# Performance work log

Measured on AMD Instinct MI355X. Metric: run time of the kernel, lower is better.

The kernel has to match this reference:

```python
import jax, jax.numpy as jnp
import numpy as np

DIM = 512
NUM_GROUPS = 32
HEADS = 16
HEAD_DIM = 32
EPS = 1e-6


def group_norm(x, w, b, num_groups=NUM_GROUPS, eps=EPS):
    # x: [B, C, H, W]
    B, C, H, W = x.shape
    xg = x.reshape(B, num_groups, -1)
    mean = xg.mean(axis=-1, keepdims=True)
    var = xg.var(axis=-1, keepdims=True)
    xg = (xg - mean) / jnp.sqrt(var + eps)
    x = xg.reshape(B, C, H, W)
    return x * w[None, :, None, None] + b[None, :, None, None]


def conv1x1(x, w, b):
    # x: [B, C, H, W], w: [O, C], b: [O]
    return jnp.einsum('bchw,oc->bohw', x, w) + b[None, :, None, None]


def setup_inputs() -> dict:
    key = jax.random.key(0)
    ks = jax.random.split(key, 12)
    s = 1.0 / np.sqrt(DIM)
    d = {
        'x': jax.random.normal(ks[0], (1, DIM, 64, 64), dtype=jnp.float32),
        'gn_w': jnp.ones((DIM,), dtype=jnp.float32),
        'gn_b': jnp.zeros((DIM,), dtype=jnp.float32),
        'wq': jax.random.normal(ks[1], (DIM, DIM), dtype=jnp.float32) * s,
        'bq': jax.random.normal(ks[2], (DIM,), dtype=jnp.float32) * 0.01,
        'wk': jax.random.normal(ks[3], (DIM, DIM), dtype=jnp.float32) * s,
        'bk': jax.random.normal(ks[4], (DIM,), dtype=jnp.float32) * 0.01,
        'wv': jax.random.normal(ks[5], (DIM, DIM), dtype=jnp.float32) * s,
        'bv': jax.random.normal(ks[6], (DIM,), dtype=jnp.float32) * 0.01,
        'wo': jax.random.normal(ks[7], (DIM, DIM), dtype=jnp.float32) * s,
        'bo': jax.random.normal(ks[8], (DIM,), dtype=jnp.float32) * 0.01,
    }
    return d


def reference(x, gn_w, gn_b, wq, bq, wk, bk, wv, bv, wo, bo):
    B, C, H, W = x.shape
    N = H * W
    scale = HEAD_DIM ** -0.5

    q_in = x
    qn = group_norm(x, gn_w, gn_b)
    # Faithful to source: v-branch applies norm_q to the already-normalized q.
    vn = group_norm(qn, gn_w, gn_b)

    q = conv1x1(qn, wq, bq)
    k = conv1x1(vn, wk, bk)
    v = conv1x1(vn, wv, bv)

    def to_tokens(t):
        # [B, C, H, W] -> [B, heads, N, head_dim]
        return t.reshape(B, HEADS, HEAD_DIM, N).transpose(0, 1, 3, 2)

    q, k, v = to_tokens(q), to_tokens(k), to_tokens(v)

    attn = jax.nn.softmax(jnp.einsum('bhnd,bhmd->bhnm', q, k) * scale, axis=-1)
    out = jnp.einsum('bhnm,bhmd->bhnd', attn, v)  # [B, heads, N, head_dim]
    out = out.transpose(0, 1, 3, 2).reshape(B, C, H, W)
    out = conv1x1(out, wo, bo)
    return (out + q_in) / jnp.sqrt(jnp.float32(2.0))
```

## Files before the change

### kernel.cpp

```cpp
#include <hip/hip_runtime.h>

#define NTOK 4096
#define CHAN 512
#define GSIZE 65536
#define RSQRT2 0.7071067811865476f
#define SCALEX 0.2550348837f
#define WB_OFF 32768
#define QT_OFF (WB_OFF + 2097152)
#define XT_OFF (QT_OFF + 4194304)
#define WS_NEEDED ((size_t)(XT_OFF + 4194304))

typedef unsigned short ushort_t;
typedef __attribute__((ext_vector_type(8))) short bf16x8;
typedef __attribute__((ext_vector_type(8))) _Float16 f16x8;
typedef __attribute__((ext_vector_type(4))) float f32x4;

__device__ __forceinline__ ushort_t f2b(float f) {
    unsigned u = __float_as_uint(f);
    unsigned r = (u + 0x7FFFu + ((u >> 16) & 1u)) >> 16;
    return (ushort_t)r;
}
__device__ __forceinline__ unsigned pack2r(float a, float b) {
    unsigned ua = __float_as_uint(a), ub = __float_as_uint(b);
    return ((ua + 0x8000u) >> 16) | ((ub + 0x8000u) & 0xFFFF0000u);
}
__device__ __forceinline__ unsigned packh2(float a, float b) {
    return __builtin_bit_cast(unsigned, __builtin_amdgcn_cvt_pkrtz(a, b));
}
__device__ __forceinline__ ushort_t f2h(float f) {
    return (ushort_t)(packh2(f, f) & 0xFFFFu);
}
__device__ __forceinline__ bf16x8 ldfrag(const ushort_t* p) {
    return __builtin_bit_cast(bf16x8, *(const uint4*)p);
}
__device__ __forceinline__ f16x8 ldfragh(const ushort_t* p) {
    return __builtin_bit_cast(f16x8, *(const uint4*)p);
}
__device__ __forceinline__ float exp2_raw(float x) {
#if __has_builtin(__builtin_amdgcn_exp2f)
    return __builtin_amdgcn_exp2f(x);
#else
    return __expf(x * 0.6931471805599453f);
#endif
}
__device__ __forceinline__ void ldg2lds16(const void* g, void* l) {
    __builtin_amdgcn_global_load_lds(
        (const __attribute__((address_space(1))) void*)g,
        (__attribute__((address_space(3))) void*)l, 16, 0, 0);
}

__global__ void diag_kernel(float* out, float v) {
    if (threadIdx.x == 0 && blockIdx.x == 0) out[0] = v;
}

__global__ __launch_bounds__(256) void gn_sums(const float* __restrict__ x,
                                               float* __restrict__ S,
                                               float* __restrict__ SS) {
    int c = blockIdx.x, t = threadIdx.x;
    const float4* p = (const float4*)(x + (size_t)c * 4096);
    float s = 0.f, ss = 0.f;
    #pragma unroll
    for (int i = 0; i < 4; i++) {
        float4 f = p[i * 256 + t];
        s += f.x + f.y + f.z + f.w;
        ss += f.x * f.x + f.y * f.y + f.z * f.z + f.w * f.w;
    }
    #pragma unroll
    for (int off = 32; off > 0; off >>= 1) {
        s += __shfl_xor(s, off);
        ss += __shfl_xor(ss, off);
    }
    __shared__ float as[4], bs[4];
    int w = t >> 6;
    if ((t & 63) == 0) { as[w] = s; bs[w] = ss; }
    __syncthreads();
    if (t == 0) {
        S[c] = as[0] + as[1] + as[2] + as[3];
        SS[c] = bs[0] + bs[1] + bs[2] + bs[3];
    }
}

__global__ __launch_bounds__(512) void gn_coef(const float* __restrict__ S,
                                               const float* __restrict__ SS,
                                               const float* __restrict__ gnw,
                                               const float* __restrict__ gnb,
                                               float* __restrict__ qa,
                                               float* __restrict__ qd,
                                               float* __restrict__ va,
                                               float* __restrict__ vd) {
    int c = threadIdx.x;
    float Sc = S[c], SSc = SS[c];
    float gs = Sc, gss = SSc;
    #pragma unroll
    for (int off = 1; off < 16; off <<= 1) {
        gs += __shfl_xor(gs, off);
        gss += __shfl_xor(gss, off);
    }
    float mu = gs * (1.f / GSIZE);
    float var = gss * (1.f / GSIZE) - mu * mu;
    float r1 = rsqrtf(var + 1e-6f);
    float wc = gnw[c], bc = gnb[c];
    float a1 = r1 * wc;
    float d1 = bc - mu * a1;
    qa[c] = a1; qd[c] = d1;
    float S2 = a1 * Sc + 4096.f * d1;
    float SS2 = a1 * a1 * SSc + 2.f * a1 * d1 * Sc + 4096.f * d1 * d1;
    float gs2 = S2, gss2 = SS2;
    #pragma unroll
    for (int off = 1; off < 16; off <<= 1) {
        gs2 += __shfl_xor(gs2, off);
        gss2 += __shfl_xor(gss2, off);
    }
    float mu2 = gs2 * (1.f / GSIZE);
    float var2 = gss2 * (1.f / GSIZE) - mu2 * mu2;
    float r2 = rsqrtf(var2 + 1e-6f);
    float a2 = r2 * wc;
    va[c] = a1 * a2;
    vd[c] = a2 * (d1 - mu2) + bc;
}

__global__ __launch_bounds__(256) void prep_all(const float* __restrict__ wq,
                                                const float* __restrict__ wk,
                                                const float* __restrict__ wv,
                                                const float* __restrict__ wo,
                                                const float* __restrict__ bq,
                                                const float* __restrict__ bk,
                                                const float* __restrict__ bv,
                                                const float* __restrict__ qa,
                                                const float* __restrict__ qd,
                                                const float* __restrict__ va,
                                                const float* __restrict__ vd,
                                                float* __restrict__ bqf,
                                                float* __restrict__ bkf,
                                                float* __restrict__ bvf,
                                                ushort_t* __restrict__ Wb) {
    int bx = blockIdx.x;
    if (bx < 384) {
        int row = bx * 4 + (threadIdx.x >> 6);
        int lane = threadIdx.x & 63;
        int m = row >> 9;
        int o = row & 511;
        const float* W = (m == 0) ? wq : (m == 1) ? wk : wv;
        const float* b = (m == 0) ? bq : (m == 1) ? bk : bv;
        const float* d = (m == 0) ? qd : vd;
        float* outp    = (m == 0) ? bqf : (m == 1) ? bkf : bvf;
        const float4* wr = (const float4*)(W + (size_t)o * 512) + lane * 2;
        const float4* dr = (const float4*)d + lane * 2;
        float4 a0 = wr[0], a1 = wr[1], d0 = dr[0], d1 = dr[1];
        float acc = a0.x * d0.x + a0.y * d0.y + a0.z * d0.z + a0.w * d0.w
                  + a1.x * d1.x + a1.y * d1.y + a1.z * d1.z + a1.w * d1.w;
        #pragma unroll
        for (int off = 32; off > 0; off >>= 1) acc += __shfl_xor(acc, off);
        if (lane == 0) outp[o] = b[o] + acc;
    } else {
        int idx = bx - 384;
        int y = idx >> 8;
        const float* src = (y == 0) ? wq : (y == 1) ? wk : (y == 2) ? wv : wo;
        int i = ((idx & 255) * 256 + threadIdx.x) * 4;
        float4 f = *(const float4*)(src + i);
        if (y < 3) {
            const float* aff = (y == 0) ? qa : va;
            float4 a = *(const float4*)(aff + (i & 511));
            f.x *= a.x; f.y *= a.y; f.z *= a.z; f.w *= a.w;
        }
        uint2 u;
        u.x = pack2r(f.x, f.y);
        u.y = pack2r(f.z, f.w);
        *(uint2*)(Wb + (size_t)y * 262144 + i) = u;
    }
}

__global__ __launch_bounds__(256) void xprep(const float* __restrict__ x,
                                             ushort_t* __restrict__ xT) {
    int bx = blockIdx.x;
    int t0 = (bx & 63) << 6;
    int c0 = (bx >> 6) << 6;
    int t = threadIdx.x;
    int tok = t & 63, c16 = t >> 6;
    float v[16];
    #pragma unroll
    for (int i = 0; i < 16; i++)
        v[i] = x[(size_t)(c0 + c16 * 16 + i) * NTOK + t0 + tok];
    uint4 u0, u1;
    u0.x = pack2r(v[0], v[1]);   u0.y = pack2r(v[2], v[3]);
    u0.z = pack2r(v[4], v[5]);   u0.w = pack2r(v[6], v[7]);
    u1.x = pack2r(v[8], v[9]);   u1.y = pack2r(v[10], v[11]);
    u1.z = pack2r(v[12], v[13]); u1.w = pack2r(v[14], v[15]);
    ushort_t* dst = xT + (size_t)(t0 + tok) * 512 + c0 + c16 * 16;
    *(uint4*)dst = u0;
    *(uint4*)(dst + 8) = u1;
}

__global__ __launch_bounds__(256) void qkv_mfma(const ushort_t* __restrict__ xT,
                                                const ushort_t* __restrict__ Wb,
                                                const float* __restrict__ bqf,
                                                const float* __restrict__ bkf,
                                                const float* __restrict__ bvf,
                                                ushort_t* __restrict__ QT,
                                                ushort_t* __restrict__ KT,
                                                ushort_t* __restrict__ Vb) {
    __shared__ __align__(16) ushort_t SH[2][12288];
    int t = threadIdx.x;
    int nbase = blockIdx.x << 6;
    int y = blockIdx.y;
    int buf = y >> 2;
    int obase = (y & 3) << 7;
    const ushort_t* Wsrc = Wb + (size_t)buf * 262144 + (size_t)obase * 512;
    const float* bias = (buf == 0) ? bqf : (buf == 1) ? bkf : bvf;

    int w = t >> 6, lane = t & 63, q15 = lane & 15, quad = lane >> 4;
    f32x4 acc[2][4];
    #pragma unroll
    for (int i = 0; i < 2; i++)
        #pragma unroll
        for (int j = 0; j < 4; j++) acc[i][j] = (f32x4){0.f, 0.f, 0.f, 0.f};

    auto issue = [&](int ck, int b) {
        ushort_t* base = SH[b];
        #pragma unroll
        for (int i = 0; i < 4; i++) {
            int idx = t + (i << 8);
            int row = idx >> 3, gs = idx & 7;
            int g = gs ^ (row & 7);
            ldg2lds16(&Wsrc[(size_t)row * 512 + ck + g * 8], &base[idx * 8]);
        }
        #pragma unroll
        for (int i = 0; i < 2; i++) {
            int idx = t + (i << 8);
            int tok = idx >> 3, gs = idx & 7;
            int g = gs ^ (tok & 7);
            ldg2lds16(&xT[(size_t)(nbase + tok) * 512 + ck + g * 8],
                      &base[8192 + idx * 8]);
        }
    };

    issue(0, 0);
    int swz = q15 & 7;
    for (int s = 0; s < 8; s++) {
        int cur = s & 1;
        __syncthreads();
        if (s < 7) issue((s + 1) * 64, cur ^ 1);
        const ushort_t* Wl = SH[cur];
        const ushort_t* Bn = SH[cur] + 8192;
        #pragma unroll
        for (int kk = 0; kk < 2; kk++) {
            int g = (kk * 4 + quad) ^ swz;
            bf16x8 af0 = ldfrag(&Wl[((w * 32 + q15) * 8 + g) * 8]);
            bf16x8 af1 = ldfrag(&Wl[((w * 32 + 16 + q15) * 8 + g) * 8]);
            #pragma unroll
            for (int n8 = 0; n8 < 4; n8++) {
                bf16x8 bfv = ldfrag(&Bn[((n8 * 16 + q15) * 8 + g) * 8]);
                acc[0][n8] = __builtin_amdgcn_mfma_f32_16x16x32_bf16(af0, bfv, acc[0][n8], 0, 0, 0);
                acc[1][n8] = __builtin_amdgcn_mfma_f32_16x16x32_bf16(af1, bfv, acc[1][n8], 0, 0, 0);
            }
        }
    }

    if (buf == 2) {
        #pragma unroll
        for (int mi = 0; mi < 2; mi++)
            #pragma unroll
            for (int r = 0; r < 4; r++) {
                int o = obase + w * 32 + mi * 16 + quad * 4 + r;
                float bo = bias[o];
                #pragma unroll
                for (int n8 = 0; n8 < 4; n8++)
                    Vb[(size_t)o * NTOK + nbase + n8 * 16 + q15] = f2h(acc[mi][n8][r] + bo);
            }
        return;
    }

    ushort_t* Tl = SH[0];
    __syncthreads();
    float qs = (buf == 0) ? SCALEX : 1.0f;
    #pragma unroll
    for (int mi = 0; mi < 2; mi++)
        #pragma unroll
        for (int r = 0; r < 4; r++) {
            int mloc = w * 32 + mi * 16 + quad * 4 + r;
            float bo = bias[obase + mloc];
            #pragma unroll
            for (int n8 = 0; n8 < 4; n8++)
                Tl[(n8 * 16 + q15) * 136 + mloc] = f2b((acc[mi][n8][r] + bo) * qs);
        }
    __syncthreads();
    ushort_t* dstT = (buf == 0) ? QT : KT;
    #pragma unroll
    for (int i = 0; i < 4; i++) {
        int idx = 4 * t + i;
        int row = idx >> 4, ch = idx & 15;
        uint4 u = *(const uint4*)&Tl[row * 136 + ch * 8];
        *(uint4*)&dstT[(size_t)(nbase + row) * 512 + obase + ch * 8] = u;
    }
}

__global__ __launch_bounds__(512, 4) void attn_v14(ushort_t* __restrict__ QT,
                                                   const ushort_t* __restrict__ KT,
                                                   const ushort_t* __restrict__ V) {
    __shared__ __align__(16) ushort_t KtF[2][8192];
    __shared__ __align__(16) ushort_t VtF[2][8192];
    int h = blockIdx.y;
    int t = threadIdx.x;
    int w = t >> 6, lane = t & 63, q15 = lane & 15, quad = lane >> 4;
    int qbase = (blockIdx.x << 7) + w * 16;
    int hc = h * 32;
    const ushort_t* Vh = V + (size_t)hc * NTOK;

    bf16x8 qf = ldfrag(&QT[(size_t)(qbase + q15) * 512 + hc + quad * 8]);

    const uint4 onesu = {0x3C003C00u, 0x3C003C00u, 0x3C003C00u, 0x3C003C00u};
    const f16x8 ones = __builtin_bit_cast(f16x8, onesu);

    f32x4 o[2] = {{0.f, 0.f, 0.f, 0.f}, {0.f, 0.f, 0.f, 0.f}};
    f32x4 lacc = {0.f, 0.f, 0.f, 0.f};

    auto issue = [&](int j0, int b) {
        #pragma unroll
        for (int i = 0; i < 2; i++) {
            int sbase = (w << 6) + (i << 9);
            int idx = sbase + lane;
            int krow = idx >> 2;
            int gd = (idx & 3) ^ ((krow >> 1) & 3);
            int rp = krow & 63;
            int srcr = (krow & 192) | (rp & 0x23) | ((rp & 0x0C) << 1) | ((rp & 0x10) >> 2);
            ldg2lds16(&KT[(size_t)(j0 + srcr) * 512 + hc + gd * 8],
                      &KtF[b][sbase * 8]);
        }
        #pragma unroll
        for (int i = 0; i < 2; i++) {
            int sbase = (w << 6) + (i << 9);
            int idx = sbase + lane;
            int d = idx >> 5;
            int gd = (idx & 31) ^ (d & 7);
            ldg2lds16(&Vh[(size_t)d * NTOK + j0 + gd * 8],
                      &VtF[b][sbase * 8]);
        }
    };

    issue(0, 0);
    int ksp8 = (quad ^ ((q15 >> 1) & 3)) * 8;
    int vq = q15 & 7;

    for (int tt = 0; tt < 16; tt++) {
        int cur = tt & 1;
        __syncthreads();
        if (tt < 15) issue((tt + 1) << 8, cur ^ 1);
        const ushort_t* KtC = KtF[cur];
        const ushort_t* VtC = VtF[cur];

        #pragma unroll
        for (int h2 = 0; h2 < 4; h2++) {
            f32x4 st[4];
            __builtin_amdgcn_s_setprio(1);
            #pragma unroll
            for (int kt = 0; kt < 4; kt++) {
                bf16x8 kf = ldfrag(&KtC[(h2 * 64 + kt * 16 + q15) * 32 + ksp8]);
                f32x4 z = {0.f, 0.f, 0.f, 0.f};
                st[kt] = __builtin_amdgcn_mfma_f32_16x16x32_bf16(kf, qf, z, 0, 0, 0);
            }
            __builtin_amdgcn_s_setprio(0);

            #pragma unroll
            for (int kt = 0; kt < 4; kt++)
                #pragma unroll
                for (int r = 0; r < 4; r++)
                    st[kt][r] = exp2_raw(st[kt][r]);

            int g0 = ((h2 * 8 + quad) ^ vq) * 8;
            int g1 = g0 ^ 32;
            f16x8 v00 = ldfragh(&VtC[q15 * 256 + g0]);
            f16x8 v01 = ldfragh(&VtC[(16 + q15) * 256 + g0]);
            f16x8 v10 = ldfragh(&VtC[q15 * 256 + g1]);
            f16x8 v11 = ldfragh(&VtC[(16 + q15) * 256 + g1]);

            uint4 p0u, p1u;
            p0u.x = packh2(st[0][0], st[0][1]);
            p0u.y = packh2(st[0][2], st[0][3]);
            p0u.z = packh2(st[1][0], st[1][1]);
            p0u.w = packh2(st[1][2], st[1][3]);
            p1u.x = packh2(st[2][0], st[2][1]);
            p1u.y = packh2(st[2][2], st[2][3]);
            p1u.z = packh2(st[3][0], st[3][1]);
            p1u.w = packh2(st[3][2], st[3][3]);
            f16x8 pf0 = __builtin_bit_cast(f16x8, p0u);
            f16x8 pf1 = __builtin_bit_cast(f16x8, p1u);
            __builtin_amdgcn_s_setprio(1);
            o[0] = __builtin_amdgcn_mfma_f32_16x16x32_f16(pf0, v00, o[0], 0, 0, 0);
            o[1] = __builtin_amdgcn_mfma_f32_16x16x32_f16(pf0, v01, o[1], 0, 0, 0);
            lacc = __builtin_amdgcn_mfma_f32_16x16x32_f16(pf0, ones, lacc, 0, 0, 0);
            o[0] = __builtin_amdgcn_mfma_f32_16x16x32_f16(pf1, v10, o[0], 0, 0, 0);
            o[1] = __builtin_amdgcn_mfma_f32_16x16x32_f16(pf1, v11, o[1], 0, 0, 0);
            lacc = __builtin_amdgcn_mfma_f32_16x16x32_f16(pf1, ones, lacc, 0, 0, 0);
            __builtin_amdgcn_s_setprio(0);
        }
    }

    #pragma unroll
    for (int r = 0; r < 4; r++) {
        float li = 1.f / lacc[r];
        int q = quad * 4 + r;
        QT[(size_t)(qbase + q) * 512 + hc + q15]      = f2b(o[0][r] * li);
        QT[(size_t)(qbase + q) * 512 + hc + 16 + q15] = f2b(o[1][r] * li);
    }
}

__global__ __launch_bounds__(256) void oproj_mfma(const ushort_t* __restrict__ OT,
                                                  const ushort_t* __restrict__ Wob,
                                                  const float* __restrict__ bo,
                                                  const float* __restrict__ x,
                                                  float* __restrict__ out) {
    __shared__ __align__(16) ushort_t Wl[64][72];
    __shared__ __align__(16) ushort_t Bn[64][72];
    int t = threadIdx.x;
    int nbase = blockIdx.x << 6;
    int obase = blockIdx.y << 6;
    int w = t >> 6, lane = t & 63, q15 = lane & 15, quad = lane >> 4;

    f32x4 acc[4];
    #pragma unroll
    for (int i = 0; i < 4; i++) acc[i] = (f32x4){0.f, 0.f, 0.f, 0.f};

    for (int ck = 0; ck < 512; ck += 64) {
        __syncthreads();
        #pragma unroll
        for (int i = 0; i < 2; i++) {
            int idx = t * 2 + i;
            int row = idx >> 3, seg = idx & 7;
            *(uint4*)&Wl[row][seg * 8] =
                *(const uint4*)&Wob[(size_t)(obase + row) * 512 + ck + seg * 8];
            *(uint4*)&Bn[row][seg * 8] =
                *(const uint4*)&OT[(size_t)(nbase + row) * 512 + ck + seg * 8];
        }
        __syncthreads();
        #pragma unroll
        for (int kk = 0; kk < 2; kk++) {
            bf16x8 af = ldfrag(&Wl[w * 16 + q15][kk * 32 + quad * 8]);
            #pragma unroll
            for (int n8 = 0; n8 < 4; n8++) {
                bf16x8 bfv = ldfrag(&Bn[n8 * 16 + q15][kk * 32 + quad * 8]);
                acc[n8] = __builtin_amdgcn_mfma_f32_16x16x32_bf16(af, bfv, acc[n8], 0, 0, 0);
            }
        }
    }

    #pragma unroll
    for (int r = 0; r < 4; r++) {
        int o = obase + w * 16 + quad * 4 + r;
        float b = bo[o];
        #pragma unroll
        for (int n8 = 0; n8 < 4; n8++) {
            size_t idx = (size_t)o * NTOK + nbase + n8 * 16 + q15;
            out[idx] = (acc[n8][r] + b + x[idx]) * RSQRT2;
        }
    }
}

extern "C" void kernel_launch(void* const* d_in, const int* in_sizes, int n_in,
                              void* d_out, int out_size, void* d_ws, size_t ws_size,
                              hipStream_t stream) {
    const float* x   = (const float*)d_in[0];
    const float* gnw = (const float*)d_in[1];
    const float* gnb = (const float*)d_in[2];
    const float* wq  = (const float*)d_in[3];
    const float* bq  = (const float*)d_in[4];
    const float* wk  = (const float*)d_in[5];
    const float* bk  = (const float*)d_in[6];
    const float* wv  = (const float*)d_in[7];
    const float* bv  = (const float*)d_in[8];
    const float* wo  = (const float*)d_in[9];
    const float* bo  = (const float*)d_in[10];
    float* out = (float*)d_out;

    if (ws_size < WS_NEEDED) {
        diag_kernel<<<1, 64, 0, stream>>>(out, (float)(ws_size >> 16));
        return;
    }

    char* wsb = (char*)d_ws;
    float* S   = (float*)(wsb + 0);
    float* SS  = (float*)(wsb + 2048);
    float* qa  = (float*)(wsb + 4096);
    float* qd  = (float*)(wsb + 6144);
    float* va  = (float*)(wsb + 8192);
    float* vd  = (float*)(wsb + 10240);
    float* bqf = (float*)(wsb + 12288);
    float* bkf = (float*)(wsb + 14336);
    float* bvf = (float*)(wsb + 16384);
    ushort_t* Wb = (ushort_t*)(wsb + WB_OFF);
    ushort_t* QT = (ushort_t*)(wsb + QT_OFF);
    ushort_t* xT = (ushort_t*)(wsb + XT_OFF);
    ushort_t* KT = (ushort_t*)d_out;
    ushort_t* Vb = (ushort_t*)d_out + (size_t)CHAN * NTOK;

    gn_sums<<<512, 256, 0, stream>>>(x, S, SS);
    gn_coef<<<1, 512, 0, stream>>>(S, SS, gnw, gnb, qa, qd, va, vd);
    prep_all<<<1408, 256, 0, stream>>>(wq, wk, wv, wo, bq, bk, bv,
                                       qa, qd, va, vd, bqf, bkf, bvf, Wb);
    xprep<<<512, 256, 0, stream>>>(x, xT);

    qkv_mfma<<<dim3(64, 12), 256, 0, stream>>>(xT, Wb, bqf, bkf, bvf, QT, KT, Vb);

    attn_v14<<<dim3(32, 16), 512, 0, stream>>>(QT, KT, Vb);

    oproj_mfma<<<dim3(64, 8), 256, 0, stream>>>(QT, Wb + (size_t)3 * 262144, bo, x, out);
}
```

Baseline: 160.8 us.

## Fuse all stages into one persistent kernel with software grid barriers

Result: slower. 611.7 us (+280.3%).

```diff
diff --git a/kernel.cpp b/kernel.cpp
--- a/kernel.cpp
+++ b/kernel.cpp
@@ -5,10 +5,12 @@
 #define GSIZE 65536
 #define RSQRT2 0.7071067811865476f
 #define SCALEX 0.2550348837f
+#define BAR_OFF 20480
 #define WB_OFF 32768
 #define QT_OFF (WB_OFF + 2097152)
 #define XT_OFF (QT_OFF + 4194304)
 #define WS_NEEDED ((size_t)(XT_OFF + 4194304))
+#define NBLK 512
 
 typedef unsigned short ushort_t;
 typedef __attribute__((ext_vector_type(8))) short bf16x8;
@@ -49,408 +51,407 @@
         (__attribute__((address_space(3))) void*)l, 16, 0, 0);
 }
 
+__device__ __forceinline__ void gridbar(unsigned* cnt, unsigned* gen) {
+    __syncthreads();
+    if (threadIdx.x == 0) {
+        __threadfence();
+        unsigned g = __hip_atomic_load(gen, __ATOMIC_ACQUIRE, __HIP_MEMORY_SCOPE_AGENT);
+        unsigned a = __hip_atomic_fetch_add(cnt, 1u, __ATOMIC_ACQ_REL, __HIP_MEMORY_SCOPE_AGENT);
+        if (a == NBLK - 1) {
+            __hip_atomic_store(cnt, 0u, __ATOMIC_RELAXED, __HIP_MEMORY_SCOPE_AGENT);
+            __hip_atomic_store(gen, g + 1u, __ATOMIC_RELEASE, __HIP_MEMORY_SCOPE_AGENT);
+        } else {
+            while (__hip_atomic_load(gen, __ATOMIC_ACQUIRE, __HIP_MEMORY_SCOPE_AGENT) == g)
+                __builtin_amdgcn_s_sleep(1);
+        }
+        __threadfence();
+    }
+    __syncthreads();
+}
+
 __global__ void diag_kernel(float* out, float v) {
     if (threadIdx.x == 0 && blockIdx.x == 0) out[0] = v;
 }
 
-__global__ __launch_bounds__(256) void gn_sums(const float* __restrict__ x,
-                                               float* __restrict__ S,
-                                               float* __restrict__ SS) {
-    int c = blockIdx.x, t = threadIdx.x;
-    const float4* p = (const float4*)(x + (size_t)c * 4096);
-    float s = 0.f, ss = 0.f;
-    #pragma unroll
-    for (int i = 0; i < 4; i++) {
-        float4 f = p[i * 256 + t];
-        s += f.x + f.y + f.z + f.w;
-        ss += f.x * f.x + f.y * f.y + f.z * f.z + f.w * f.w;
-    }
-    #pragma unroll
-    for (int off = 32; off > 0; off >>= 1) {
-        s += __shfl_xor(s, off);
-        ss += __shfl_xor(ss, off);
-    }
-    __shared__ float as[4], bs[4];
-    int w = t >> 6;
-    if ((t & 63) == 0) { as[w] = s; bs[w] = ss; }
-    __syncthreads();
-    if (t == 0) {
-        S[c] = as[0] + as[1] + as[2] + as[3];
-        SS[c] = bs[0] + bs[1] + bs[2] + bs[3];
-    }
-}
-
-__global__ __launch_bounds__(512) void gn_coef(const float* __restrict__ S,
-                                               const float* __restrict__ SS,
+__global__ __launch_bounds__(512, 4) void mega(const float* __restrict__ x,
                                                const float* __restrict__ gnw,
                                                const float* __restrict__ gnb,
-                                               float* __restrict__ qa,
-                                               float* __restrict__ qd,
-                                               float* __restrict__ va,
-                                               float* __restrict__ vd) {
-    int c = threadIdx.x;
-    float Sc = S[c], SSc = SS[c];
-    float gs = Sc, gss = SSc;
-    #pragma unroll
-    for (int off = 1; off < 16; off <<= 1) {
-        gs += __shfl_xor(gs, off);
-        gss += __shfl_xor(gss, off);
-    }
-    float mu = gs * (1.f / GSIZE);
-    float var = gss * (1.f / GSIZE) - mu * mu;
-    float r1 = rsqrtf(var + 1e-6f);
-    float wc = gnw[c], bc = gnb[c];
-    float a1 = r1 * wc;
-    float d1 = bc - mu * a1;
-    qa[c] = a1; qd[c] = d1;
-    float S2 = a1 * Sc + 4096.f * d1;
-    float SS2 = a1 * a1 * SSc + 2.f * a1 * d1 * Sc + 4096.f * d1 * d1;
-    float gs2 = S2, gss2 = SS2;
-    #pragma unroll
-    for (int off = 1; off < 16; off <<= 1) {
-        gs2 += __shfl_xor(gs2, off);
-        gss2 += __shfl_xor(gss2, off);
-    }
-    float mu2 = gs2 * (1.f / GSIZE);
-    float var2 = gss2 * (1.f / GSIZE) - mu2 * mu2;
-    float r2 = rsqrtf(var2 + 1e-6f);
-    float a2 = r2 * wc;
-    va[c] = a1 * a2;
-    vd[c] = a2 * (d1 - mu2) + bc;
-}
-
-__global__ __launch_bounds__(256) void prep_all(const float* __restrict__ wq,
-                                                const float* __restrict__ wk,
-                                                const float* __restrict__ wv,
-                                                const float* __restrict__ wo,
-                                                const float* __restrict__ bq,
-                                                const float* __restrict__ bk,
-                                                const float* __restrict__ bv,
-                                                const float* __restrict__ qa,
-                                                const float* __restrict__ qd,
-                                                const float* __restrict__ va,
-                                                const float* __restrict__ vd,
-                                                float* __restrict__ bqf,
-                                                float* __restrict__ bkf,
-                                                float* __restrict__ bvf,
-                                                ushort_t* __restrict__ Wb) {
-    int bx = blockIdx.x;
-    if (bx < 384) {
-        int row = bx * 4 + (threadIdx.x >> 6);
-        int lane = threadIdx.x & 63;
-        int m = row >> 9;
-        int o = row & 511;
-        const float* W = (m == 0) ? wq : (m == 1) ? wk : wv;
-        const float* b = (m == 0) ? bq : (m == 1) ? bk : bv;
-        const float* d = (m == 0) ? qd : vd;
-        float* outp    = (m == 0) ? bqf : (m == 1) ? bkf : bvf;
-        const float4* wr = (const float4*)(W + (size_t)o * 512) + lane * 2;
-        const float4* dr = (const float4*)d + lane * 2;
-        float4 a0 = wr[0], a1 = wr[1], d0 = dr[0], d1 = dr[1];
-        float acc = a0.x * d0.x + a0.y * d0.y + a0.z * d0.z + a0.w * d0.w
-                  + a1.x * d1.x + a1.y * d1.y + a1.z * d1.z + a1.w * d1.w;
-        #pragma unroll
-        for (int off = 32; off > 0; off >>= 1) acc += __shfl_xor(acc, off);
-        if (lane == 0) outp[o] = b[o] + acc;
-    } else {
-        int idx = bx - 384;
-        int y = idx >> 8;
-        const float* src = (y == 0) ? wq : (y == 1) ? wk : (y == 2) ? wv : wo;
-        int i = ((idx & 255) * 256 + threadIdx.x) * 4;
-        float4 f = *(const float4*)(src + i);
-        if (y < 3) {
-            const float* aff = (y == 0) ? qa : va;
-            float4 a = *(const float4*)(aff + (i & 511));
-            f.x *= a.x; f.y *= a.y; f.z *= a.z; f.w *= a.w;
-        }
-        uint2 u;
-        u.x = pack2r(f.x, f.y);
-        u.y = pack2r(f.z, f.w);
-        *(uint2*)(Wb + (size_t)y * 262144 + i) = u;
-    }
-}
-
-__global__ __launch_bounds__(256) void xprep(const float* __restrict__ x,
-                                             ushort_t* __restrict__ xT) {
-    int bx = blockIdx.x;
-    int t0 = (bx & 63) << 6;
-    int c0 = (bx >> 6) << 6;
-    int t = threadIdx.x;
-    int tok = t & 63, c16 = t >> 6;
-    float v[16];
-    #pragma unroll
-    for (int i = 0; i < 16; i++)
-        v[i] = x[(size_t)(c0 + c16 * 16 + i) * NTOK + t0 + tok];
-    uint4 u0, u1;
-    u0.x = pack2r(v[0], v[1]);   u0.y = pack2r(v[2], v[3]);
-    u0.z = pack2r(v[4], v[5]);   u0.w = pack2r(v[6], v[7]);
-    u1.x = pack2r(v[8], v[9]);   u1.y = pack2r(v[10], v[11]);
-    u1.z = pack2r(v[12], v[13]); u1.w = pack2r(v[14], v[15]);
-    ushort_t* dst = xT + (size_t)(t0 + tok) * 512 + c0 + c16 * 16;
-    *(uint4*)dst = u0;
-    *(uint4*)(dst + 8) = u1;
-}
-
-__global__ __launch_bounds__(256) void qkv_mfma(const ushort_t* __restrict__ xT,
-                                                const ushort_t* __restrict__ Wb,
-                                                const float* __restrict__ bqf,
-                                                const float* __restrict__ bkf,
-                                                const float* __restrict__ bvf,
-                                                ushort_t* __restrict__ QT,
-                                                ushort_t* __restrict__ KT,
-                                                ushort_t* __restrict__ Vb) {
-    __shared__ __align__(16) ushort_t SH[2][12288];
-    int t = threadIdx.x;
-    int nbase = blockIdx.x << 6;
-    int y = blockIdx.y;
-    int buf = y >> 2;
-    int obase = (y & 3) << 7;
-    const ushort_t* Wsrc = Wb + (size_t)buf * 262144 + (size_t)obase * 512;
-    const float* bias = (buf == 0) ? bqf : (buf == 1) ? bkf : bvf;
-
+                                               const float* __restrict__ wq,
+                                               const float* __restrict__ bq,
+                                               const float* __restrict__ wk,
+                                               const float* __restrict__ bk,
+                                               const float* __restrict__ wv,
+                                               const float* __restrict__ bv,
+                                               const float* __restrict__ wo,
+                                               const float* __restrict__ bo,
+                                               char* __restrict__ wsb,
+                                               float* __restrict__ out) {
+    __shared__ __align__(16) char SM[65536];
+    int b = blockIdx.x, t = threadIdx.x;
     int w = t >> 6, lane = t & 63, q15 = lane & 15, quad = lane >> 4;
-    f32x4 acc[2][4];
-    #pragma unroll
-    for (int i = 0; i < 2; i++)
-        #pragma unroll
-        for (int j = 0; j < 4; j++) acc[i][j] = (f32x4){0.f, 0.f, 0.f, 0.f};
-
-    auto issue = [&](int ck, int b) {
-        ushort_t* base = SH[b];
-        #pragma unroll
-        for (int i = 0; i < 4; i++) {
-            int idx = t + (i << 8);
-            int row = idx >> 3, gs = idx & 7;
-            int g = gs ^ (row & 7);
-            ldg2lds16(&Wsrc[(size_t)row * 512 + ck + g * 8], &base[idx * 8]);
-        }
-        #pragma unroll
-        for (int i = 0; i < 2; i++) {
-            int idx = t + (i << 8);
-            int tok = idx >> 3, gs = idx & 7;
-            int g = gs ^ (tok & 7);
-            ldg2lds16(&xT[(size_t)(nbase + tok) * 512 + ck + g * 8],
-                      &base[8192 + idx * 8]);
-        }
-    };
-
-    issue(0, 0);
-    int swz = q15 & 7;
-    for (int s = 0; s < 8; s++) {
-        int cur = s & 1;
+
+    float* S   = (float*)(wsb + 0);
+    float* SS  = (float*)(wsb + 2048);
+    float* bqf = (float*)(wsb + 12288);
+    float* bkf = (float*)(wsb + 14336);
+    float* bvf = (float*)(wsb + 16384);
+    unsigned* cnt = (unsigned*)(wsb + BAR_OFF);
+    unsigned* gen = cnt + 1;
+    ushort_t* Wb = (ushort_t*)(wsb + WB_OFF);
+    ushort_t* QT = (ushort_t*)(wsb + QT_OFF);
+    ushort_t* xT = (ushort_t*)(wsb + XT_OFF);
+    ushort_t* KT = (ushort_t*)out;
+    ushort_t* Vb = (ushort_t*)out + (size_t)CHAN * NTOK;
+
+    {
+        const float4* p = (const float4*)(x + (size_t)b * 4096);
+        float4 f1 = p[t], f2 = p[t + 512];
+        float s = f1.x + f1.y + f1.z + f1.w + f2.x + f2.y + f2.z + f2.w;
+        float ss = f1.x * f1.x + f1.y * f1.y + f1.z * f1.z + f1.w * f1.w
+                 + f2.x * f2.x + f2.y * f2.y + f2.z * f2.z + f2.w * f2.w;
+        #pragma unroll
+        for (int off = 32; off > 0; off >>= 1) {
+            s += __shfl_xor(s, off);
+            ss += __shfl_xor(ss, off);
+        }
+        float* red = (float*)SM;
+        if (lane == 0) { red[w] = s; red[8 + w] = ss; }
         __syncthreads();
-        if (s < 7) issue((s + 1) * 64, cur ^ 1);
-        const ushort_t* Wl = SH[cur];
-        const ushort_t* Bn = SH[cur] + 8192;
-        #pragma unroll
-        for (int kk = 0; kk < 2; kk++) {
-            int g = (kk * 4 + quad) ^ swz;
-            bf16x8 af0 = ldfrag(&Wl[((w * 32 + q15) * 8 + g) * 8]);
-            bf16x8 af1 = ldfrag(&Wl[((w * 32 + 16 + q15) * 8 + g) * 8]);
+        if (t == 0) {
+            float a = 0.f, c2 = 0.f;
+            #pragma unroll
+            for (int i = 0; i < 8; i++) { a += red[i]; c2 += red[8 + i]; }
+            S[b] = a; SS[b] = c2;
+        }
+        int t0 = (b & 63) << 6;
+        int c0 = (b >> 6) << 6;
+        int tok = t & 63, c8 = t >> 6;
+        float v[8];
+        #pragma unroll
+        for (int i = 0; i < 8; i++)
+            v[i] = x[(size_t)(c0 + c8 * 8 + i) * NTOK + t0 + tok];
+        uint4 u;
+        u.x = pack2r(v[0], v[1]); u.y = pack2r(v[2], v[3]);
+        u.z = pack2r(v[4], v[5]); u.w = pack2r(v[6], v[7]);
+        *(uint4*)&xT[(size_t)(t0 + tok) * 512 + c0 + c8 * 8] = u;
+    }
+    gridbar(cnt, gen);
+
+    {
+        float* qaL = (float*)SM;
+        float* qdL = qaL + 512;
+        float* vaL = qaL + 1024;
+        float* vdL = qaL + 1536;
+        {
+            int c = t;
+            float Sc = S[c], SSc = SS[c];
+            float gs = Sc, gss = SSc;
+            #pragma unroll
+            for (int off = 1; off < 16; off <<= 1) {
+                gs += __shfl_xor(gs, off);
+                gss += __shfl_xor(gss, off);
+            }
+            float mu = gs * (1.f / GSIZE);
+            float var = gss * (1.f / GSIZE) - mu * mu;
+            float r1 = rsqrtf(var + 1e-6f);
+            float wc = gnw[c], bc = gnb[c];
+            float a1 = r1 * wc;
+            float d1 = bc - mu * a1;
+            float S2 = a1 * Sc + 4096.f * d1;
+            float SS2 = a1 * a1 * SSc + 2.f * a1 * d1 * Sc + 4096.f * d1 * d1;
+            float gs2 = S2, gss2 = SS2;
+            #pragma unroll
+            for (int off = 1; off < 16; off <<= 1) {
+                gs2 += __shfl_xor(gs2, off);
+                gss2 += __shfl_xor(gss2, off);
+            }
+            float mu2 = gs2 * (1.f / GSIZE);
+            float var2 = gss2 * (1.f / GSIZE) - mu2 * mu2;
+            float r2 = rsqrtf(var2 + 1e-6f);
+            float a2 = r2 * wc;
+            qaL[c] = a1; qdL[c] = d1;
+            vaL[c] = a1 * a2;
+            vdL[c] = a2 * (d1 - mu2) + bc;
+        }
+        __syncthreads();
+        auto do_unit = [&](int u) {
+            if (u < 192) {
+                int row = u * 8 + w;
+                int m = row >> 9;
+                int o = row & 511;
+                const float* W = (m == 0) ? wq : (m == 1) ? wk : wv;
+                const float* bb = (m == 0) ? bq : (m == 1) ? bk : bv;
+                const float* d = (m == 0) ? qdL : vdL;
+                float* outp = (m == 0) ? bqf : (m == 1) ? bkf : bvf;
+                const float4* wr = (const float4*)(W + (size_t)o * 512) + lane * 2;
+                float4 a0 = wr[0], a1 = wr[1];
+                float4 d0 = *(const float4*)&d[lane * 8];
+                float4 d1 = *(const float4*)&d[lane * 8 + 4];
+                float acc = a0.x * d0.x + a0.y * d0.y + a0.z * d0.z + a0.w * d0.w
+                          + a1.x * d1.x + a1.y * d1.y + a1.z * d1.z + a1.w * d1.w;
+                #pragma unroll
+                for (int off = 32; off > 0; off >>= 1) acc += __shfl_xor(acc, off);
+                if (lane == 0) outp[o] = bb[o] + acc;
+            } else {
+                int k = u - 192;
+                int y = k >> 7;
+                const float* src = (y == 0) ? wq : (y == 1) ? wk : (y == 2) ? wv : wo;
+                int i = (k & 127) * 2048 + t * 4;
+                float4 f = *(const float4*)(src + i);
+                if (y < 3) {
+                    const float* aff = (y == 0) ? qaL : vaL;
+                    int c = i & 511;
+                    f.x *= aff[c]; f.y *= aff[c + 1]; f.z *= aff[c + 2]; f.w *= aff[c + 3];
+                }
+                uint2 uu;
+                uu.x = pack2r(f.x, f.y);
+                uu.y = pack2r(f.z, f.w);
+                *(uint2*)(Wb + (size_t)y * 262144 + i) = uu;
+            }
+        };
+        do_unit(b);
+        if (b < 192) do_unit(b + 512);
+    }
+    gridbar(cnt, gen);
+
+    if (b < 384) {
+        ushort_t* SH = (ushort_t*)SM;
+        int nbase = (b & 31) << 7;
+        int y = b >> 5;
+        int buf = y >> 2;
+        int obase = (y & 3) << 7;
+        const ushort_t* Wsrc = Wb + (size_t)buf * 262144 + (size_t)obase * 512;
+        const float* bias = (buf == 0) ? bqf : (buf == 1) ? bkf : bvf;
+
+        f32x4 acc[8];
+        #pragma unroll
+        for (int i = 0; i < 8; i++) acc[i] = (f32x4){0.f, 0.f, 0.f, 0.f};
+
+        auto issue = [&](int ck, int bb) {
+            ushort_t* base = SH + bb * 16384;
+            #pragma unroll
+            for (int i = 0; i < 2; i++) {
+                int idx = t + (i << 9);
+                int row = idx >> 3, gs = idx & 7;
+                int g = gs ^ (row & 7);
+                ldg2lds16(&Wsrc[(size_t)row * 512 + ck + g * 8], &base[idx * 8]);
+            }
+            #pragma unroll
+            for (int i = 0; i < 2; i++) {
+                int idx = t + (i << 9);
+                int tok = idx >> 3, gs = idx & 7;
+                int g = gs ^ (tok & 7);
+                ldg2lds16(&xT[(size_t)(nbase + tok) * 512 + ck + g * 8],
+                          &base[8192 + idx * 8]);
+            }
+        };
+        issue(0, 0);
+        int swz = q15 & 7;
+        for (int s = 0; s < 8; s++) {
+            int cur = s & 1;
+            __syncthreads();
+            if (s < 7) issue((s + 1) * 64, cur ^ 1);
+            const ushort_t* Wl = SH + cur * 16384;
+            const ushort_t* Bn = Wl + 8192;
+            #pragma unroll
+            for (int kk = 0; kk < 2; kk++) {
+                int g = (kk * 4 + quad) ^ swz;
+                bf16x8 af = ldfrag(&Wl[((w * 16 + q15) * 8 + g) * 8]);
+                #pragma unroll
+                for (int n8 = 0; n8 < 8; n8++) {
+                    bf16x8 bfv = ldfrag(&Bn[((n8 * 16 + q15) * 8 + g) * 8]);
+                    acc[n8] = __builtin_amdgcn_mfma_f32_16x16x32_bf16(af, bfv, acc[n8], 0, 0, 0);
+                }
+            }
+        }
+        if (buf == 2) {
+            #pragma unroll
+            for (int r = 0; r < 4; r++) {
+                int o = obase + w * 16 + quad * 4 + r;
+                float bo_ = bias[o];
+                #pragma unroll
+                for (int n8 = 0; n8 < 8; n8++)
+                    Vb[(size_t)o * NTOK + nbase + n8 * 16 + q15] = f2h(acc[n8][r] + bo_);
+            }
+        } else {
+            ushort_t* Tl = (ushort_t*)SM;
+            __syncthreads();
+            float qs = (buf == 0) ? SCALEX : 1.0f;
+            #pragma unroll
+            for (int r = 0; r < 4; r++) {
+                int mloc = w * 16 + quad * 4 + r;
+                float bo_ = bias[obase + mloc];
+                #pragma unroll
+                for (int n8 = 0; n8 < 8; n8++)
+                    Tl[(n8 * 16 + q15) * 136 + mloc] = f2b((acc[n8][r] + bo_) * qs);
+            }
+            __syncthreads();
+            ushort_t* dstT = (buf == 0) ? QT : KT;
+            #pragma unroll
+            for (int i = 0; i < 4; i++) {
+                int idx = 4 * t + i;
+                int row = idx >> 4, ch = idx & 15;
+                uint4 u = *(const uint4*)&Tl[row * 136 + ch * 8];
+                *(uint4*)&dstT[(size_t)(nbase + row) * 512 + obase + ch * 8] = u;
+            }
+        }
+    }
+    gridbar(cnt, gen);
+
+    {
+        ushort_t (*KtF)[8192] = (ushort_t(*)[8192])SM;
+        ushort_t (*VtF)[8192] = (ushort_t(*)[8192])(SM + 32768);
+        int h = b >> 5;
+        int qbase = ((b & 31) << 7) + w * 16;
+        int hc = h * 32;
+        const ushort_t* Vh = Vb + (size_t)hc * NTOK;
+
+        bf16x8 qf = ldfrag(&QT[(size_t)(qbase + q15) * 512 + hc + quad * 8]);
+
+        const uint4 onesu = {0x3C003C00u, 0x3C003C00u, 0x3C003C00u, 0x3C003C00u};
+        const f16x8 ones = __builtin_bit_cast(f16x8, onesu);
+
+        f32x4 o[2] = {{0.f, 0.f, 0.f, 0.f}, {0.f, 0.f, 0.f, 0.f}};
+        f32x4 lacc = {0.f, 0.f, 0.f, 0.f};
+
+        auto issue = [&](int j0, int bb) {
+            #pragma unroll
+            for (int i = 0; i < 2; i++) {
+                int sbase = (w << 6) + (i << 9);
+                int idx = sbase + lane;
+                int krow = idx >> 2;
+                int gd = (idx & 3) ^ ((krow >> 1) & 3);
+                int rp = krow & 63;
+                int srcr = (krow & 192) | (rp & 0x23) | ((rp & 0x0C) << 1) | ((rp & 0x10) >> 2);
+                ldg2lds16(&KT[(size_t)(j0 + srcr) * 512 + hc + gd * 8],
+                          &KtF[bb][sbase * 8]);
+            }
+            #pragma unroll
+            for (int i = 0; i < 2; i++) {
+                int sbase = (w << 6) + (i << 9);
+                int idx = sbase + lane;
+                int d = idx >> 5;
+                int gd = (idx & 31) ^ (d & 7);
+                ldg2lds16(&Vh[(size_t)d * NTOK + j0 + gd * 8],
+                          &VtF[bb][sbase * 8]);
+            }
+        };
+
+        issue(0, 0);
+        int ksp8 = (quad ^ ((q15 >> 1) & 3)) * 8;
+        int vq = q15 & 7;
+
+        for (int tt = 0; tt < 16; tt++) {
+            int cur = tt & 1;
+            __syncthreads();
+            if (tt < 15) issue((tt + 1) << 8, cur ^ 1);
+            const ushort_t* KtC = KtF[cur];
+            const ushort_t* VtC = VtF[cur];
+
+            #pragma unroll
+            for (int h2 = 0; h2 < 4; h2++) {
+                f32x4 st[4];
+                __builtin_amdgcn_s_setprio(1);
+                #pragma unroll
+                for (int kt = 0; kt < 4; kt++) {
+                    bf16x8 kf = ldfrag(&KtC[(h2 * 64 + kt * 16 + q15) * 32 + ksp8]);
+                    f32x4 z = {0.f, 0.f, 0.f, 0.f};
+                    st[kt] = __builtin_amdgcn_mfma_f32_16x16x32_bf16(kf, qf, z, 0, 0, 0);
+                }
+                __builtin_amdgcn_s_setprio(0);
+
+                #pragma unroll
+                for (int kt = 0; kt < 4; kt++)
+                    #pragma unroll
+                    for (int r = 0; r < 4; r++)
+                        st[kt][r] = exp2_raw(st[kt][r]);
+
+                int g0 = ((h2 * 8 + quad) ^ vq) * 8;
+                int g1 = g0 ^ 32;
+                f16x8 v00 = ldfragh(&VtC[q15 * 256 + g0]);
+                f16x8 v01 = ldfragh(&VtC[(16 + q15) * 256 + g0]);
+                f16x8 v10 = ldfragh(&VtC[q15 * 256 + g1]);
+                f16x8 v11 = ldfragh(&VtC[(16 + q15) * 256 + g1]);
+
+                uint4 p0u, p1u;
+                p0u.x = packh2(st[0][0], st[0][1]);
+                p0u.y = packh2(st[0][2], st[0][3]);
+                p0u.z = packh2(st[1][0], st[1][1]);
+                p0u.w = packh2(st[1][2], st[1][3]);
+                p1u.x = packh2(st[2][0], st[2][1]);
+                p1u.y = packh2(st[2][2], st[2][3]);
+                p1u.z = packh2(st[3][0], st[3][1]);
+                p1u.w = packh2(st[3][2], st[3][3]);
+                f16x8 pf0 = __builtin_bit_cast(f16x8, p0u);
+                f16x8 pf1 = __builtin_bit_cast(f16x8, p1u);
+                __builtin_amdgcn_s_setprio(1);
+                o[0] = __builtin_amdgcn_mfma_f32_16x16x32_f16(pf0, v00, o[0], 0, 0, 0);
+                o[1] = __builtin_amdgcn_mfma_f32_16x16x32_f16(pf0, v01, o[1], 0, 0, 0);
+                lacc = __builtin_amdgcn_mfma_f32_16x16x32_f16(pf0, ones, lacc, 0, 0, 0);
+                o[0] = __builtin_amdgcn_mfma_f32_16x16x32_f16(pf1, v10, o[0], 0, 0, 0);
+                o[1] = __builtin_amdgcn_mfma_f32_16x16x32_f16(pf1, v11, o[1], 0, 0, 0);
+                lacc = __builtin_amdgcn_mfma_f32_16x16x32_f16(pf1, ones, lacc, 0, 0, 0);
+                __builtin_amdgcn_s_setprio(0);
+            }
+        }
+
+        #pragma unroll
+        for (int r = 0; r < 4; r++) {
+            float li = 1.f / lacc[r];
+            int q = quad * 4 + r;
+            QT[(size_t)(qbase + q) * 512 + hc + q15]      = f2b(o[0][r] * li);
+            QT[(size_t)(qbase + q) * 512 + hc + 16 + q15] = f2b(o[1][r] * li);
+        }
+    }
+    gridbar(cnt, gen);
+
+    if (b < 256) {
+        ushort_t* Wl = (ushort_t*)SM;
+        ushort_t* Bn = (ushort_t*)SM + 4608;
+        const ushort_t* Wob = Wb + (size_t)3 * 262144;
+        int nbase = (b & 31) << 7;
+        int obase = (b >> 5) << 6;
+        int w4 = w & 3, nh = w >> 2;
+
+        f32x4 acc[4];
+        #pragma unroll
+        for (int i = 0; i < 4; i++) acc[i] = (f32x4){0.f, 0.f, 0.f, 0.f};
+
+        for (int ck = 0; ck < 512; ck += 64) {
+            __syncthreads();
+            {
+                int row = t >> 3, seg = t & 7;
+                *(uint4*)&Wl[(row * 72) + seg * 8] =
+                    *(const uint4*)&Wob[(size_t)(obase + row) * 512 + ck + seg * 8];
+            }
+            #pragma unroll
+            for (int i = 0; i < 2; i++) {
+                int idx = t + (i << 9);
+                int row = idx >> 3, seg = idx & 7;
+                *(uint4*)&Bn[(row * 72) + seg * 8] =
+                    *(const uint4*)&QT[(size_t)(nbase + row) * 512 + ck + seg * 8];
+            }
+            __syncthreads();
+            #pragma unroll
+            for (int kk = 0; kk < 2; kk++) {
+                bf16x8 af = ldfrag(&Wl[(w4 * 16 + q15) * 72 + kk * 32 + quad * 8]);
+                #pragma unroll
+                for (int n8 = 0; n8 < 4; n8++) {
+                    bf16x8 bfv = ldfrag(&Bn[(nh * 64 + n8 * 16 + q15) * 72 + kk * 32 + quad * 8]);
+                    acc[n8] = __builtin_amdgcn_mfma_f32_16x16x32_bf16(af, bfv, acc[n8], 0, 0, 0);
+                }
+            }
+        }
+
+        #pragma unroll
+        for (int r = 0; r < 4; r++) {
+            int o = obase + w4 * 16 + quad * 4 + r;
+            float bb = bo[o];
             #pragma unroll
             for (int n8 = 0; n8 < 4; n8++) {
-                bf16x8 bfv = ldfrag(&Bn[((n8 * 16 + q15) * 8 + g) * 8]);
-                acc[0][n8] = __builtin_amdgcn_mfma_f32_16x16x32_bf16(af0, bfv, acc[0][n8], 0, 0, 0);
-                acc[1][n8] = __builtin_amdgcn_mfma_f32_16x16x32_bf16(af1, bfv, acc[1][n8], 0, 0, 0);
-            }
-        }
-    }
-
-    if (buf == 2) {
-        #pragma unroll
-        for (int mi = 0; mi < 2; mi++)
-            #pragma unroll
-            for (int r = 0; r < 4; r++) {
-                int o = obase + w * 32 + mi * 16 + quad * 4 + r;
-                float bo = bias[o];
-                #pragma unroll
-                for (int n8 = 0; n8 < 4; n8++)
-                    Vb[(size_t)o * NTOK + nbase + n8 * 16 + q15] = f2h(acc[mi][n8][r] + bo);
-            }
-        return;
-    }
-
-    ushort_t* Tl = SH[0];
-    __syncthreads();
-    float qs = (buf == 0) ? SCALEX : 1.0f;
-    #pragma unroll
-    for (int mi = 0; mi < 2; mi++)
-        #pragma unroll
-        for (int r = 0; r < 4; r++) {
-            int mloc = w * 32 + mi * 16 + quad * 4 + r;
-            float bo = bias[obase + mloc];
-            #pragma unroll
-            for (int n8 = 0; n8 < 4; n8++)
-                Tl[(n8 * 16 + q15) * 136 + mloc] = f2b((acc[mi][n8][r] + bo) * qs);
-        }
-    __syncthreads();
-    ushort_t* dstT = (buf == 0) ? QT : KT;
-    #pragma unroll
-    for (int i = 0; i < 4; i++) {
-        int idx = 4 * t + i;
-        int row = idx >> 4, ch = idx & 15;
-        uint4 u = *(const uint4*)&Tl[row * 136 + ch * 8];
-        *(uint4*)&dstT[(size_t)(nbase + row) * 512 + obase + ch * 8] = u;
-    }
-}
-
-__global__ __launch_bounds__(512, 4) void attn_v14(ushort_t* __restrict__ QT,
-                                                   const ushort_t* __restrict__ KT,
-                                                   const ushort_t* __restrict__ V) {
-    __shared__ __align__(16) ushort_t KtF[2][8192];
-    __shared__ __align__(16) ushort_t VtF[2][8192];
-    int h = blockIdx.y;
-    int t = threadIdx.x;
-    int w = t >> 6, lane = t & 63, q15 = lane & 15, quad = lane >> 4;
-    int qbase = (blockIdx.x << 7) + w * 16;
-    int hc = h * 32;
-    const ushort_t* Vh = V + (size_t)hc * NTOK;
-
-    bf16x8 qf = ldfrag(&QT[(size_t)(qbase + q15) * 512 + hc + quad * 8]);
-
-    const uint4 onesu = {0x3C003C00u, 0x3C003C00u, 0x3C003C00u, 0x3C003C00u};
-    const f16x8 ones = __builtin_bit_cast(f16x8, onesu);
-
-    f32x4 o[2] = {{0.f, 0.f, 0.f, 0.f}, {0.f, 0.f, 0.f, 0.f}};
-    f32x4 lacc = {0.f, 0.f, 0.f, 0.f};
-
-    auto issue = [&](int j0, int b) {
-        #pragma unroll
-        for (int i = 0; i < 2; i++) {
-            int sbase = (w << 6) + (i << 9);
-            int idx = sbase + lane;
-            int krow = idx >> 2;
-            int gd = (idx & 3) ^ ((krow >> 1) & 3);
-            int rp = krow & 63;
-            int srcr = (krow & 192) | (rp & 0x23) | ((rp & 0x0C) << 1) | ((rp & 0x10) >> 2);
-            ldg2lds16(&KT[(size_t)(j0 + srcr) * 512 + hc + gd * 8],
-                      &KtF[b][sbase * 8]);
-        }
-        #pragma unroll
-        for (int i = 0; i < 2; i++) {
-            int sbase = (w << 6) + (i << 9);
-            int idx = sbase + lane;
-            int d = idx >> 5;
-            int gd = (idx & 31) ^ (d & 7);
-            ldg2lds16(&Vh[(size_t)d * NTOK + j0 + gd * 8],
-                      &VtF[b][sbase * 8]);
-        }
-    };
-
-    issue(0, 0);
-    int ksp8 = (quad ^ ((q15 >> 1) & 3)) * 8;
-    int vq = q15 & 7;
-
-    for (int tt = 0; tt < 16; tt++) {
-        int cur = tt & 1;
-        __syncthreads();
-        if (tt < 15) issue((tt + 1) << 8, cur ^ 1);
-        const ushort_t* KtC = KtF[cur];
-        const ushort_t* VtC = VtF[cur];
-
-        #pragma unroll
-        for (int h2 = 0; h2 < 4; h2++) {
-            f32x4 st[4];
-            __builtin_amdgcn_s_setprio(1);
-            #pragma unroll
-            for (int kt = 0; kt < 4; kt++) {
-                bf16x8 kf = ldfrag(&KtC[(h2 * 64 + kt * 16 + q15) * 32 + ksp8]);
-                f32x4 z = {0.f, 0.f, 0.f, 0.f};
-                st[kt] = __builtin_amdgcn_mfma_f32_16x16x32_bf16(kf, qf, z, 0, 0, 0);
-            }
-            __builtin_amdgcn_s_setprio(0);
-
-            #pragma unroll
-            for (int kt = 0; kt < 4; kt++)
-                #pragma unroll
-                for (int r = 0; r < 4; r++)
-                    st[kt][r] = exp2_raw(st[kt][r]);
-
-            int g0 = ((h2 * 8 + quad) ^ vq) * 8;
-            int g1 = g0 ^ 32;
-            f16x8 v00 = ldfragh(&VtC[q15 * 256 + g0]);
-            f16x8 v01 = ldfragh(&VtC[(16 + q15) * 256 + g0]);
-            f16x8 v10 = ldfragh(&VtC[q15 * 256 + g1]);
-            f16x8 v11 = ldfragh(&VtC[(16 + q15) * 256 + g1]);
-
-            uint4 p0u, p1u;
-            p0u.x = packh2(st[0][0], st[0][1]);
-            p0u.y = packh2(st[0][2], st[0][3]);
-            p0u.z = packh2(st[1][0], st[1][1]);
-            p0u.w = packh2(st[1][2], st[1][3]);
-            p1u.x = packh2(st[2][0], st[2][1]);
-            p1u.y = packh2(st[2][2], st[2][3]);
-            p1u.z = packh2(st[3][0], st[3][1]);
-            p1u.w = packh2(st[3][2], st[3][3]);
-            f16x8 pf0 = __builtin_bit_cast(f16x8, p0u);
-            f16x8 pf1 = __builtin_bit_cast(f16x8, p1u);
-            __builtin_amdgcn_s_setprio(1);
-            o[0] = __builtin_amdgcn_mfma_f32_16x16x32_f16(pf0, v00, o[0], 0, 0, 0);
-            o[1] = __builtin_amdgcn_mfma_f32_16x16x32_f16(pf0, v01, o[1], 0, 0, 0);
-            lacc = __builtin_amdgcn_mfma_f32_16x16x32_f16(pf0, ones, lacc, 0, 0, 0);
-            o[0] = __builtin_amdgcn_mfma_f32_16x16x32_f16(pf1, v10, o[0], 0, 0, 0);
-            o[1] = __builtin_amdgcn_mfma_f32_16x16x32_f16(pf1, v11, o[1], 0, 0, 0);
-            lacc = __builtin_amdgcn_mfma_f32_16x16x32_f16(pf1, ones, lacc, 0, 0, 0);
-            __builtin_amdgcn_s_setprio(0);
-        }
-    }
-
-    #pragma unroll
-    for (int r = 0; r < 4; r++) {
-        float li = 1.f / lacc[r];
-        int q = quad * 4 + r;
-        QT[(size_t)(qbase + q) * 512 + hc + q15]      = f2b(o[0][r] * li);
-        QT[(size_t)(qbase + q) * 512 + hc + 16 + q15] = f2b(o[1][r] * li);
-    }
-}
-
-__global__ __launch_bounds__(256) void oproj_mfma(const ushort_t* __restrict__ OT,
-                                                  const ushort_t* __restrict__ Wob,
-                                                  const float* __restrict__ bo,
-                                                  const float* __restrict__ x,
-                                                  float* __restrict__ out) {
-    __shared__ __align__(16) ushort_t Wl[64][72];
-    __shared__ __align__(16) ushort_t Bn[64][72];
-    int t = threadIdx.x;
-    int nbase = blockIdx.x << 6;
-    int obase = blockIdx.y << 6;
-    int w = t >> 6, lane = t & 63, q15 = lane & 15, quad = lane >> 4;
-
-    f32x4 acc[4];
-    #pragma unroll
-    for (int i = 0; i < 4; i++) acc[i] = (f32x4){0.f, 0.f, 0.f, 0.f};
-
-    for (int ck = 0; ck < 512; ck += 64) {
-        __syncthreads();
-        #pragma unroll
-        for (int i = 0; i < 2; i++) {
-            int idx = t * 2 + i;
-            int row = idx >> 3, seg = idx & 7;
-            *(uint4*)&Wl[row][seg * 8] =
-                *(const uint4*)&Wob[(size_t)(obase + row) * 512 + ck + seg * 8];
-            *(uint4*)&Bn[row][seg * 8] =
-                *(const uint4*)&OT[(size_t)(nbase + row) * 512 + ck + seg * 8];
-        }
-        __syncthreads();
-        #pragma unroll
-        for (int kk = 0; kk < 2; kk++) {
-            bf16x8 af = ldfrag(&Wl[w * 16 + q15][kk * 32 + quad * 8]);
-            #pragma unroll
-            for (int n8 = 0; n8 < 4; n8++) {
-                bf16x8 bfv = ldfrag(&Bn[n8 * 16 + q15][kk * 32 + quad * 8]);
-                acc[n8] = __builtin_amdgcn_mfma_f32_16x16x32_bf16(af, bfv, acc[n8], 0, 0, 0);
-            }
-        }
-    }
-
-    #pragma unroll
-    for (int r = 0; r < 4; r++) {
-        int o = obase + w * 16 + quad * 4 + r;
-        float b = bo[o];
-        #pragma unroll
-        for (int n8 = 0; n8 < 4; n8++) {
-            size_t idx = (size_t)o * NTOK + nbase + n8 * 16 + q15;
-            out[idx] = (acc[n8][r] + b + x[idx]) * RSQRT2;
+                size_t idx = (size_t)o * NTOK + nbase + nh * 64 + n8 * 16 + q15;
+                out[idx] = (acc[n8][r] + bb + x[idx]) * RSQRT2;
+            }
         }
     }
 }
@@ -477,30 +478,7 @@
     }
 
     char* wsb = (char*)d_ws;
-    float* S   = (float*)(wsb + 0);
-    float* SS  = (float*)(wsb + 2048);
-    float* qa  = (float*)(wsb + 4096);
-    float* qd  = (float*)(wsb + 6144);
-    float* va  = (float*)(wsb + 8192);
-    float* vd  = (float*)(wsb + 10240);
-    float* bqf = (float*)(wsb + 12288);
-    float* bkf = (float*)(wsb + 14336);
-    float* bvf = (float*)(wsb + 16384);
-    ushort_t* Wb = (ushort_t*)(wsb + WB_OFF);
-    ushort_t* QT = (ushort_t*)(wsb + QT_OFF);
-    ushort_t* xT = (ushort_t*)(wsb + XT_OFF);
-    ushort_t* KT = (ushort_t*)d_out;
-    ushort_t* Vb = (ushort_t*)d_out + (size_t)CHAN * NTOK;
-
-    gn_sums<<<512, 256, 0, stream>>>(x, S, SS);
-    gn_coef<<<1, 512, 0, stream>>>(S, SS, gnw, gnb, qa, qd, va, vd);
-    prep_all<<<1408, 256, 0, stream>>>(wq, wk, wv, wo, bq, bk, bv,
-                                       qa, qd, va, vd, bqf, bkf, bvf, Wb);
-    xprep<<<512, 256, 0, stream>>>(x, xT);
-
-    qkv_mfma<<<dim3(64, 12), 256, 0, stream>>>(xT, Wb, bqf, bkf, bvf, QT, KT, Vb);
-
-    attn_v14<<<dim3(32, 16), 512, 0, stream>>>(QT, KT, Vb);
-
-    oproj_mfma<<<dim3(64, 8), 256, 0, stream>>>(QT, Wb + (size_t)3 * 262144, bo, x, out);
-}
+    hipMemsetAsync(wsb + BAR_OFF, 0, 8, stream);
+    mega<<<NBLK, 512, 0, stream>>>(x, gnw, gnb, wq, bq, wk, bk, wv, bv, wo, bo,
+                                   wsb, out);
+}
```
